# Optimization experiments

Hardware: AMD Instinct MI355X
Metric: run time of the kernel (lower is better)

## Reference

```python
import jax, jax.numpy as jnp
import numpy as np
import math

SEQ_LEN = 1024
NUM_FILTERS = 24
INPUT_DIM = 256
OUTPUT_DIM = 256
BATCH = 4


def _spectral_filters(seq_len, K):
    # Hankel matrix Z[i,j] = 2 / ((i+j)^3 - (i+j)), i,j in 1..L (use_hankel_L=False)
    entries = np.arange(1, seq_len + 1, dtype=np.float64)
    ipj = entries[:, None] + entries[None, :]
    Z = 2.0 / (ipj ** 3 - ipj)
    sigma, phi = np.linalg.eigh(Z)
    phi_k = phi[:, -K:] * (sigma[-K:] ** 0.25)
    return jnp.asarray(phi_k, dtype=jnp.float32)  # [L, K]


def setup_inputs() -> dict:
    key = jax.random.key(0)
    k1, k2, k3 = jax.random.split(key, 3)
    scale = (NUM_FILTERS * INPUT_DIM) ** (-0.5)
    x = jax.random.normal(k1, (BATCH, SEQ_LEN, INPUT_DIM), dtype=jnp.float32)
    phi = _spectral_filters(SEQ_LEN, NUM_FILTERS)
    M_phi_plus = jax.random.normal(k2, (NUM_FILTERS, INPUT_DIM, OUTPUT_DIM), dtype=jnp.float32) * scale
    M_phi_minus = jax.random.normal(k3, (NUM_FILTERS, INPUT_DIM, OUTPUT_DIM), dtype=jnp.float32) * scale
    return {"x": x, "phi": phi, "M_phi_plus": M_phi_plus, "M_phi_minus": M_phi_minus}


def reference(x, phi, M_phi_plus, M_phi_minus):
    B, L, I = x.shape
    n = 1 << math.ceil(math.log2(2 * L - 1))  # FFT length (2048 for L=1024)
    # alternating sign: +1 at even positions, -1 at odd (sgn[:,1::2] *= -1)
    sgn = jnp.where(jnp.arange(L) % 2 == 1, -1.0, 1.0).astype(jnp.float32)
    # FFT of filters: [F, K]
    V = jnp.fft.rfft(phi.astype(jnp.float32), n=n, axis=0)
    # FFT of input and sign-modulated input: [B, F, I]
    X = jnp.fft.rfft(x, n=n, axis=1)
    Xs = jnp.fft.rfft(x * sgn[None, :, None], n=n, axis=1)
    # pointwise multiply in frequency, broadcast over K: [B, F, K, I]
    U_plus = jnp.fft.irfft(V[None, :, :, None] * X[:, :, None, :], n=n, axis=1)[:, :L]
    U_minus = jnp.fft.irfft(V[None, :, :, None] * Xs[:, :, None, :], n=n, axis=1)[:, :L]
    U_minus = U_minus * sgn[None, :, None, None]
    # spectral projection: [B, L, O]
    out = jnp.einsum('blki,kio->blo', U_plus, M_phi_plus)
    out = out + jnp.einsum('blki,kio->blo', U_minus, M_phi_minus)
    return out
```

## Files before the change

### kernel.cpp

```cpp
#include <hip/hip_runtime.h>


#define ZB_ 12582912

typedef __attribute__((ext_vector_type(8))) short bf16x8;
typedef __attribute__((ext_vector_type(4))) float f32x4;

__device__ inline unsigned short f2bf(float f) {
    unsigned u = __float_as_uint(f);
    u += 0x7FFFu + ((u >> 16) & 1u);
    return (unsigned short)(u >> 16);
}

__device__ inline float bf2f(unsigned short s) {
    unsigned u = ((unsigned)s) << 16;
    return __uint_as_float(u);
}

__device__ inline void gl16(const unsigned short* g, unsigned short* l) {
    __builtin_amdgcn_global_load_lds((const __attribute__((address_space(1))) void*)g,
                                     (__attribute__((address_space(3))) void*)l, 16, 0, 0);
}

__global__ __launch_bounds__(256) void k_prep_all(const float* __restrict__ x,
                                                  const float* __restrict__ phi,
                                                  const float* __restrict__ Mp,
                                                  const float* __restrict__ Mm,
                                                  unsigned short* __restrict__ xb,
                                                  unsigned short* __restrict__ ToepA,
                                                  unsigned short* __restrict__ MbT) {
    __shared__ float tile[32][33];
    int bid = blockIdx.x, tid = threadIdx.x;
    if (bid < 1024) {
        int i = (bid * 256 + tid) * 4;
        float4 v = *(const float4*)(x + i);
        ushort4 o;
        o.x = f2bf(v.x); o.y = f2bf(v.y); o.z = f2bf(v.z); o.w = f2bf(v.w);
        int row = i >> 8, col = i & 255;
        int dst = (row << 8) | (col & 224) | ((col & 31) ^ (((row >> 1) & 3) << 3));
        *(ushort4*)(xb + dst) = o;
    } else if (bid < 1792) {
        int r = bid - 1024;
        int kk = r >> 4;
        int dm = (r & 15) - 1;
        int k = (kk < 24) ? kk : kk - 24;
        int i = tid >> 1, j0 = (tid & 1) * 32;
        unsigned short* dst = ToepA + ((size_t)kk * 16 + (dm + 1)) * 8192 + i * 64;
        int sw = (i & 7) << 3;
#pragma unroll
        for (int q = 0; q < 8; ++q) {
            int j = j0 + q * 4;
            unsigned short e[4];
#pragma unroll
            for (int ee = 0; ee < 4; ++ee) {
                int t = dm * 64 + i - (j + ee);
                float v = 0.f;
                if (t >= 0 && t < 1024) {
                    v = phi[t * 24 + k];
                    if (kk >= 24 && (t & 1)) v = -v;
                }
                e[ee] = f2bf(v);
            }
            ushort4 ov; ov.x = e[0]; ov.y = e[1]; ov.z = e[2]; ov.w = e[3];
            *(ushort4*)(dst + (j ^ sw)) = ov;
        }
    } else {
        int flat = bid - 1792;
        int kk = flat >> 6, rr = flat & 63;
        int i0 = (rr >> 3) * 32, o0 = (rr & 7) * 32;
        int tx = tid & 31, ty = tid >> 5;
        const float* src = ((kk < 24) ? Mp : Mm) + (size_t)((kk < 24) ? kk : kk - 24) * 65536;
        for (int j = 0; j < 4; ++j)
            tile[ty + j * 8][tx] = src[(i0 + ty + j * 8) * 256 + o0 + tx];
        __syncthreads();
        for (int j = 0; j < 4; ++j) {
            int orow = o0 + ty + j * 8, i = i0 + tx;
            int ic = (i & 224) | ((i & 31) ^ (((orow >> 1) & 3) << 3));
            MbT[(size_t)kk * 65536 + orow * 256 + ic] = f2bf(tile[tx][ty + j * 8]);
        }
    }
}

__global__ __launch_bounds__(256, 4) void k_stage1(const unsigned short* __restrict__ xb0,
                                                   const unsigned short* __restrict__ MbT,
                                                   unsigned short* __restrict__ Z) {
    __shared__ unsigned short Ab[2][4096];
    __shared__ unsigned short Bb[3][4096];
    int tid = threadIdx.x, lane = tid & 63, w = tid >> 6;
    int wm = w >> 1, wn = w & 1;

    int nwg = 768 * gridDim.z;
    int orig = blockIdx.x + blockIdx.y * 8 + blockIdx.z * 768;
    int wg = (orig & 7) * (nwg >> 3) + (orig >> 3);
    int m0 = (wg & 7) * 128;
    int rem = wg >> 3;
    int yy = rem % 96;
    int b  = rem / 96;
    int kk = yy >> 1;
    int o0 = (yy & 1) * 128;

    const unsigned short* xb_b = xb0 + (size_t)b * 262144;
    unsigned short* Zb = Z + (size_t)b * ZB_;
    const unsigned short* Bsrc = MbT + (size_t)kk * 65536;
    int l16 = lane & 15, kofs = (lane >> 4) * 8;
    int sw32 = ((l16 >> 1) & 3) << 3;
    int r4l = lane >> 2, c4 = (lane & 3) * 8;

    int arow[2], brow[2], lofs[2];
#pragma unroll
    for (int q = 0; q < 2; ++q) {
        int rr = q * 64 + w * 16 + r4l;
        arow[q] = (m0 + rr) * 256 + c4;
        brow[q] = (o0 + rr) * 256 + c4;
        lofs[q] = q * 2048 + w * 512;
    }

    f32x4 acc[4][4];
    for (int i = 0; i < 4; ++i)
        for (int j = 0; j < 4; ++j) {
            acc[i][j][0] = 0.f; acc[i][j][1] = 0.f; acc[i][j][2] = 0.f; acc[i][j][3] = 0.f;
        }

    auto stageA = [&](int bi, int ko) {
#pragma unroll
        for (int q = 0; q < 2; ++q) gl16(xb_b + arow[q] + ko * 32, &Ab[bi][0] + lofs[q]);
    };
    auto stageB = [&](int bi, int ko) {
#pragma unroll
        for (int q = 0; q < 2; ++q) gl16(Bsrc + brow[q] + ko * 32, &Bb[bi][0] + lofs[q]);
    };

    stageA(0, 0); stageB(0, 0); stageB(1, 1);

    for (int ko = 0; ko < 8; ++ko) {
        if (ko < 7) { asm volatile("s_waitcnt vmcnt(2)" ::: "memory"); }
        else        { asm volatile("s_waitcnt vmcnt(0)" ::: "memory"); }
        __builtin_amdgcn_sched_barrier(0);
        __builtin_amdgcn_s_barrier();
        __builtin_amdgcn_sched_barrier(0);
        if (ko < 7) stageA((ko + 1) & 1, ko + 1);
        if (ko < 6) stageB((ko + 2) % 3, ko + 2);

        const unsigned short* Abase = &Ab[ko & 1][0];
        const unsigned short* Bbase = &Bb[ko % 3][0];
        int koX = kofs ^ sw32;
        bf16x8 af[4], bfv[4];
#pragma unroll
        for (int mi = 0; mi < 4; ++mi)
            af[mi] = *(const bf16x8*)(Abase + (wm * 64 + mi * 16 + l16) * 32 + koX);
#pragma unroll
        for (int ni = 0; ni < 4; ++ni)
            bfv[ni] = *(const bf16x8*)(Bbase + (wn * 64 + ni * 16 + l16) * 32 + koX);
        __builtin_amdgcn_s_setprio(1);
#pragma unroll
        for (int mi = 0; mi < 4; ++mi)
#pragma unroll
            for (int ni = 0; ni < 4; ++ni)
                acc[mi][ni] = __builtin_amdgcn_mfma_f32_16x16x32_bf16(af[mi], bfv[ni], acc[mi][ni], 0, 0, 0);
        __builtin_amdgcn_s_setprio(0);
    }

    int r4 = (lane >> 4) * 4;
    for (int mi = 0; mi < 4; ++mi) {
        int sbase = m0 + wm * 64 + mi * 16 + r4;
        for (int ni = 0; ni < 4; ++ni) {
            int o = o0 + wn * 64 + ni * 16 + l16;
            ushort4 pk;
            pk.x = f2bf(acc[mi][ni][0]); pk.y = f2bf(acc[mi][ni][1]);
            pk.z = f2bf(acc[mi][ni][2]); pk.w = f2bf(acc[mi][ni][3]);
            *(ushort4*)(Zb + (size_t)kk * 262144 + (size_t)o * 1024 + (sbase ^ ((o & 7) << 3))) = pk;
        }
    }
}

__global__ __launch_bounds__(256, 2) void k_stage2(const unsigned short* __restrict__ Z,
                                                   const unsigned short* __restrict__ ToepA,
                                                   unsigned short* __restrict__ partial, int kkpg) {
    __shared__ unsigned short Abuf[2][8192];
    __shared__ unsigned short Zbuf[3][8192];
    int tid = threadIdx.x, lane = tid & 63, w = tid >> 6;
    int wm = w >> 1, wn = w & 1;

    int gy = gridDim.y, nwg = 4 * gy * gridDim.z;
    int orig = blockIdx.x + blockIdx.y * 4 + blockIdx.z * 4 * gy;
    int wg = (orig & 7) * (nwg >> 3) + (orig >> 3);
    int pr = wg & 3;
    int yy = (wg >> 2) % gy;
    int zz = (wg >> 2) / gy;
    int o0 = (yy & 1) * 128;
    int b  = yy >> 1;
    int kgi = zz;
    int kk0 = kgi * kkpg;

    int l16 = lane & 15, kofs = (lane >> 4) * 8;
    int sw = (l16 & 7) << 3;
    int r8 = lane >> 3, cg = lane & 7;

    const unsigned short* Zb = Z + (size_t)b * ZB_;
    unsigned short* pb = partial + ((size_t)b * gridDim.z + kgi) * 262144;

    int arow[4], zrow[4], lofs[4];
#pragma unroll
    for (int q = 0; q < 4; ++q) {
        int rr = q * 32 + w * 8 + r8;
        arow[q] = rr * 64 + cg * 8;
        zrow[q] = (o0 + rr) * 1024 + cg * 8;
        lofs[q] = q * 2048 + w * 512;
    }

    for (int half = 0; half < 2; ++half) {
        int lb = half ? (7 - pr) : pr;
        int l0 = lb * 128;
        int nch = 2 * lb + 2;
        int total = kkpg * nch;

        f32x4 acc[4][4];
        for (int i = 0; i < 4; ++i)
            for (int j = 0; j < 4; ++j) {
                acc[i][j][0] = 0.f; acc[i][j][1] = 0.f; acc[i][j][2] = 0.f; acc[i][j][3] = 0.f;
            }

        __syncthreads();

        auto stageA = [&](int bi, int kka, int didx) {
            const unsigned short* gA = ToepA + ((size_t)kka * 16 + didx) * 8192;
#pragma unroll
            for (int q = 0; q < 4; ++q) gl16(gA + arow[q], &Abuf[bi][0] + lofs[q]);
        };
        auto stageZ = [&](int bi, int kka, int s0) {
            const unsigned short* gZ = Zb + (size_t)kka * 262144 + s0;
#pragma unroll
            for (int q = 0; q < 4; ++q) gl16(gZ + zrow[q], &Zbuf[bi][0] + lofs[q]);
        };
        auto compute = [&](int ba, int bz) {
            const unsigned short* Abase = &Abuf[ba][0];
            const unsigned short* Zbase = &Zbuf[bz][0];
            __builtin_amdgcn_s_setprio(1);
#pragma unroll
            for (int ks = 0; ks < 2; ++ks) {
                int koX = (ks * 32 + kofs) ^ sw;
                bf16x8 af[4], bfv[4];
#pragma unroll
                for (int mi = 0; mi < 4; ++mi)
                    af[mi] = *(const bf16x8*)(Abase + (wm * 64 + mi * 16 + l16) * 64 + koX);
#pragma unroll
                for (int ni = 0; ni < 4; ++ni)
                    bfv[ni] = *(const bf16x8*)(Zbase + (wn * 64 + ni * 16 + l16) * 64 + koX);
#pragma unroll
                for (int mi = 0; mi < 4; ++mi)
#pragma unroll
                    for (int ni = 0; ni < 4; ++ni)
                        acc[mi][ni] = __builtin_amdgcn_mfma_f32_16x16x32_bf16(af[mi], bfv[ni], acc[mi][ni], 0, 0, 0);
            }
            __builtin_amdgcn_s_setprio(0);
        };

        stageA(0, kk0, 2 * lb + 1);
        stageZ(0, kk0, 0);
        stageZ(1, kk0, 64);

        int scA = 1, kkA = 0;
        int scZ = 2, kkZ = 0;
        if (scZ == nch) { scZ = 0; kkZ = 1; }
        int jz = 2;

        for (int j = 0; j < total - 1; ++j) {
            asm volatile("s_waitcnt vmcnt(4)" ::: "memory");
            __builtin_amdgcn_sched_barrier(0);
            __builtin_amdgcn_s_barrier();
            __builtin_amdgcn_sched_barrier(0);
            stageA((j + 1) & 1, kk0 + kkA, 2 * lb - scA + 1);
            ++scA; if (scA == nch) { scA = 0; ++kkA; }
            if (jz < total) {
                stageZ(jz % 3, kk0 + kkZ, scZ * 64);
                ++scZ; if (scZ == nch) { scZ = 0; ++kkZ; }
                ++jz;
            }
            compute(j & 1, j % 3);
        }
        asm volatile("s_waitcnt vmcnt(0)" ::: "memory");
        __builtin_amdgcn_sched_barrier(0);
        __builtin_amdgcn_s_barrier();
        __builtin_amdgcn_sched_barrier(0);
        compute((total - 1) & 1, (total - 1) % 3);

        int r4 = (lane >> 4) * 4;
        for (int mi = 0; mi < 4; ++mi) {
            int l = l0 + wm * 64 + mi * 16 + r4;
            for (int ni = 0; ni < 4; ++ni) {
                int o = o0 + wn * 64 + ni * 16 + l16;
                unsigned short* dst = pb + (size_t)l * 256 + o;
                dst[0]   = f2bf(acc[mi][ni][0]);
                dst[256] = f2bf(acc[mi][ni][1]);
                dst[512] = f2bf(acc[mi][ni][2]);
                dst[768] = f2bf(acc[mi][ni][3]);
            }
        }
    }
}

__global__ void k_reduce(const unsigned short* __restrict__ partial, float* __restrict__ outg, int kg) {
    const unsigned short* pb = partial + (size_t)blockIdx.y * kg * 262144;
    int i = (blockIdx.x * 256 + threadIdx.x) * 8;
    float s[8];
#pragma unroll
    for (int j = 0; j < 8; ++j) s[j] = 0.f;
    for (int kgi = 0; kgi < kg; ++kgi) {
        uint4 v = *(const uint4*)(pb + (size_t)kgi * 262144 + i);
        unsigned vv[4] = {v.x, v.y, v.z, v.w};
#pragma unroll
        for (int q = 0; q < 4; ++q) {
            s[q * 2]     += bf2f((unsigned short)(vv[q] & 0xFFFF));
            s[q * 2 + 1] += bf2f((unsigned short)(vv[q] >> 16));
        }
    }
    float4 o0, o1;
    o0.x = s[0]; o0.y = s[1]; o0.z = s[2]; o0.w = s[3];
    o1.x = s[4]; o1.y = s[5]; o1.z = s[6]; o1.w = s[7];
    float* dst = outg + (size_t)blockIdx.y * 262144 + i;
    *(float4*)(dst) = o0;
    *(float4*)(dst + 4) = o1;
}

extern "C" void kernel_launch(void* const* d_in, const int* in_sizes, int n_in,
                              void* d_out, int out_size, void* d_ws, size_t ws_size,
                              hipStream_t stream) {
    const float* x   = (const float*)d_in[0];
    const float* phi = (const float*)d_in[1];
    const float* Mp  = (const float*)d_in[2];
    const float* Mm  = (const float*)d_in[3];
    float* out = (float*)d_out;

    char* ws = (char*)d_ws;
    unsigned short* xb    = (unsigned short*)(ws);
    unsigned short* MbT   = (unsigned short*)(ws + 2097152);
    unsigned short* ToepA = (unsigned short*)(ws + 8388608);
    unsigned short* Zbuf  = (unsigned short*)(ws + 20971520);
    const size_t fixed = 20971520;

    int g = 4, kg = 16;
    auto need = [&](int gg, int kk) {
        return fixed + (size_t)gg * 25165824 + (size_t)gg * (size_t)kk * 524288;
    };
    if (need(4, 16) > ws_size) {
        kg = 12;
        if (need(4, 12) > ws_size) {
            g = 2; kg = 16;
            if (need(2, 16) > ws_size) {
                kg = 12;
                if (need(2, 12) > ws_size) {
                    g = 1; kg = 16;
                    if (need(1, 16) > ws_size) {
                        kg = 12;
                        if (need(1, 12) > ws_size) kg = 6;
                    }
                }
            }
        }
    }
    unsigned short* partial = (unsigned short*)(ws + fixed + (size_t)g * 25165824);

    k_prep_all<<<dim3(4864), dim3(256), 0, stream>>>(x, phi, Mp, Mm, xb, ToepA, MbT);

    for (int b0 = 0; b0 < 4; b0 += g) {
        k_stage1<<<dim3(8, 96, g), dim3(256), 0, stream>>>(xb + (size_t)b0 * 262144, MbT, Zbuf);
        k_stage2<<<dim3(4, 2 * g, kg), dim3(256), 0, stream>>>(Zbuf, ToepA, partial, 48 / kg);
        k_reduce<<<dim3(128, g), dim3(256), 0, stream>>>(partial, out + (size_t)b0 * 262144, kg);
    }
}
```

Baseline: 130.7 us.

## Halve stage-2 K-chunk to 32 with new swizzle, raise occupancy and split-K

The Toeplitz filter blocks are rebuilt as 128x32 tiles at 32-sample diagonal offsets, replacing the 128x64 tiles. The Z layout swizzle is changed to match, and stage 2 now streams 32-wide K chunks with half the LDS per buffer. This allows 4 workgroups per CU instead of 2, and the default split-K count rises from 16 to 24. The aim is higher occupancy, finer-grained triangular work and more parallelism, at the cost of more barriers per unit of work and more partial-sum traffic in the reduce step.

```diff
diff --git a/kernel.cpp b/kernel.cpp
--- a/kernel.cpp
+++ b/kernel.cpp
@@ -39,25 +39,27 @@
         int row = i >> 8, col = i & 255;
         int dst = (row << 8) | (col & 224) | ((col & 31) ^ (((row >> 1) & 3) << 3));
         *(ushort4*)(xb + dst) = o;
-    } else if (bid < 1792) {
+    } else if (bid < 2560) {
         int r = bid - 1024;
-        int kk = r >> 4;
-        int dm = (r & 15) - 1;
+        int kk = r >> 5;
+        int didx = r & 31;
+        int d = 32 * didx - 96;
         int k = (kk < 24) ? kk : kk - 24;
-        int i = tid >> 1, j0 = (tid & 1) * 32;
-        unsigned short* dst = ToepA + ((size_t)kk * 16 + (dm + 1)) * 8192 + i * 64;
-        int sw = (i & 7) << 3;
-#pragma unroll
-        for (int q = 0; q < 8; ++q) {
+        bool neg = kk >= 24;
+        int i = tid >> 1, j0 = (tid & 1) * 16;
+        unsigned short* dst = ToepA + ((size_t)kk * 32 + didx) * 4096 + i * 32;
+        int sw = ((i >> 1) & 3) << 3;
+#pragma unroll
+        for (int q = 0; q < 4; ++q) {
             int j = j0 + q * 4;
             unsigned short e[4];
 #pragma unroll
             for (int ee = 0; ee < 4; ++ee) {
-                int t = dm * 64 + i - (j + ee);
+                int t = d + i - (j + ee);
                 float v = 0.f;
                 if (t >= 0 && t < 1024) {
                     v = phi[t * 24 + k];
-                    if (kk >= 24 && (t & 1)) v = -v;
+                    if (neg && (t & 1)) v = -v;
                 }
                 e[ee] = f2bf(v);
             }
@@ -65,7 +67,7 @@
             *(ushort4*)(dst + (j ^ sw)) = ov;
         }
     } else {
-        int flat = bid - 1792;
+        int flat = bid - 2560;
         int kk = flat >> 6, rr = flat & 63;
         int i0 = (rr >> 3) * 32, o0 = (rr & 7) * 32;
         int tx = tid & 31, ty = tid >> 5;
@@ -161,23 +163,26 @@
     }
 
     int r4 = (lane >> 4) * 4;
+    int swo = 0;
     for (int mi = 0; mi < 4; ++mi) {
         int sbase = m0 + wm * 64 + mi * 16 + r4;
         for (int ni = 0; ni < 4; ++ni) {
             int o = o0 + wn * 64 + ni * 16 + l16;
+            swo = ((o >> 1) & 3) << 3;
+            int sidx = (sbase & ~31) | ((sbase & 31) ^ swo);
             ushort4 pk;
             pk.x = f2bf(acc[mi][ni][0]); pk.y = f2bf(acc[mi][ni][1]);
             pk.z = f2bf(acc[mi][ni][2]); pk.w = f2bf(acc[mi][ni][3]);
-            *(ushort4*)(Zb + (size_t)kk * 262144 + (size_t)o * 1024 + (sbase ^ ((o & 7) << 3))) = pk;
-        }
-    }
-}
-
-__global__ __launch_bounds__(256, 2) void k_stage2(const unsigned short* __restrict__ Z,
+            *(ushort4*)(Zb + (size_t)kk * 262144 + (size_t)o * 1024 + sidx) = pk;
+        }
+    }
+}
+
+__global__ __launch_bounds__(256, 4) void k_stage2(const unsigned short* __restrict__ Z,
                                                    const unsigned short* __restrict__ ToepA,
                                                    unsigned short* __restrict__ partial, int kkpg) {
-    __shared__ unsigned short Abuf[2][8192];
-    __shared__ unsigned short Zbuf[3][8192];
+    __shared__ unsigned short Abuf[2][4096];
+    __shared__ unsigned short Zbuf[3][4096];
     int tid = threadIdx.x, lane = tid & 63, w = tid >> 6;
     int wm = w >> 1, wn = w & 1;
 
@@ -193,25 +198,18 @@
     int kk0 = kgi * kkpg;
 
     int l16 = lane & 15, kofs = (lane >> 4) * 8;
-    int sw = (l16 & 7) << 3;
-    int r8 = lane >> 3, cg = lane & 7;
+    int koX = kofs ^ (((l16 >> 1) & 3) << 3);
 
     const unsigned short* Zb = Z + (size_t)b * ZB_;
     unsigned short* pb = partial + ((size_t)b * gridDim.z + kgi) * 262144;
 
-    int arow[4], zrow[4], lofs[4];
-#pragma unroll
-    for (int q = 0; q < 4; ++q) {
-        int rr = q * 32 + w * 8 + r8;
-        arow[q] = rr * 64 + cg * 8;
-        zrow[q] = (o0 + rr) * 1024 + cg * 8;
-        lofs[q] = q * 2048 + w * 512;
-    }
+    int t8 = tid * 8;
+    int zr = (tid >> 2) * 1024 + (tid & 3) * 8;
 
     for (int half = 0; half < 2; ++half) {
         int lb = half ? (7 - pr) : pr;
         int l0 = lb * 128;
-        int nch = 2 * lb + 2;
+        int nch = 4 * lb + 4;
         int total = kkpg * nch;
 
         f32x4 acc[4][4];
@@ -222,57 +220,52 @@
 
         __syncthreads();
 
-        auto stageA = [&](int bi, int kka, int didx) {
-            const unsigned short* gA = ToepA + ((size_t)kka * 16 + didx) * 8192;
-#pragma unroll
-            for (int q = 0; q < 4; ++q) gl16(gA + arow[q], &Abuf[bi][0] + lofs[q]);
+        auto stageA = [&](int bi, int kka, int sc) {
+            const unsigned short* gA = ToepA + ((size_t)kka * 32 + (4 * lb - sc + 3)) * 4096;
+            gl16(gA + t8, &Abuf[bi][0] + t8);
+            gl16(gA + 2048 + t8, &Abuf[bi][0] + 2048 + t8);
         };
-        auto stageZ = [&](int bi, int kka, int s0) {
-            const unsigned short* gZ = Zb + (size_t)kka * 262144 + s0;
-#pragma unroll
-            for (int q = 0; q < 4; ++q) gl16(gZ + zrow[q], &Zbuf[bi][0] + lofs[q]);
+        auto stageZ = [&](int bi, int kka, int sc) {
+            const unsigned short* gZ = Zb + (size_t)kka * 262144 + (size_t)o0 * 1024 + sc * 32;
+            gl16(gZ + zr, &Zbuf[bi][0] + t8);
+            gl16(gZ + 65536 + zr, &Zbuf[bi][0] + 2048 + t8);
         };
         auto compute = [&](int ba, int bz) {
             const unsigned short* Abase = &Abuf[ba][0];
             const unsigned short* Zbase = &Zbuf[bz][0];
+            bf16x8 af[4], bfv[4];
+#pragma unroll
+            for (int mi = 0; mi < 4; ++mi)
+                af[mi] = *(const bf16x8*)(Abase + (wm * 64 + mi * 16 + l16) * 32 + koX);
+#pragma unroll
+            for (int ni = 0; ni < 4; ++ni)
+                bfv[ni] = *(const bf16x8*)(Zbase + (wn * 64 + ni * 16 + l16) * 32 + koX);
             __builtin_amdgcn_s_setprio(1);
 #pragma unroll
-            for (int ks = 0; ks < 2; ++ks) {
-                int koX = (ks * 32 + kofs) ^ sw;
-                bf16x8 af[4], bfv[4];
-#pragma unroll
-                for (int mi = 0; mi < 4; ++mi)
-                    af[mi] = *(const bf16x8*)(Abase + (wm * 64 + mi * 16 + l16) * 64 + koX);
+            for (int mi = 0; mi < 4; ++mi)
 #pragma unroll
                 for (int ni = 0; ni < 4; ++ni)
-                    bfv[ni] = *(const bf16x8*)(Zbase + (wn * 64 + ni * 16 + l16) * 64 + koX);
-#pragma unroll
-                for (int mi = 0; mi < 4; ++mi)
-#pragma unroll
-                    for (int ni = 0; ni < 4; ++ni)
-                        acc[mi][ni] = __builtin_amdgcn_mfma_f32_16x16x32_bf16(af[mi], bfv[ni], acc[mi][ni], 0, 0, 0);
-            }
+                    acc[mi][ni] = __builtin_amdgcn_mfma_f32_16x16x32_bf16(af[mi], bfv[ni], acc[mi][ni], 0, 0, 0);
             __builtin_amdgcn_s_setprio(0);
         };
 
-        stageA(0, kk0, 2 * lb + 1);
+        stageA(0, kk0, 0);
         stageZ(0, kk0, 0);
-        stageZ(1, kk0, 64);
+        stageZ(1, kk0, 1);
 
         int scA = 1, kkA = 0;
         int scZ = 2, kkZ = 0;
-        if (scZ == nch) { scZ = 0; kkZ = 1; }
         int jz = 2;
 
         for (int j = 0; j < total - 1; ++j) {
-            asm volatile("s_waitcnt vmcnt(4)" ::: "memory");
+            asm volatile("s_waitcnt vmcnt(2)" ::: "memory");
             __builtin_amdgcn_sched_barrier(0);
             __builtin_amdgcn_s_barrier();
             __builtin_amdgcn_sched_barrier(0);
-            stageA((j + 1) & 1, kk0 + kkA, 2 * lb - scA + 1);
+            stageA((j + 1) & 1, kk0 + kkA, scA);
             ++scA; if (scA == nch) { scA = 0; ++kkA; }
             if (jz < total) {
-                stageZ(jz % 3, kk0 + kkZ, scZ * 64);
+                stageZ(jz % 3, kk0 + kkZ, scZ);
                 ++scZ; if (scZ == nch) { scZ = 0; ++kkZ; }
                 ++jz;
             }
@@ -338,21 +331,24 @@
     unsigned short* Zbuf  = (unsigned short*)(ws + 20971520);
     const size_t fixed = 20971520;
 
-    int g = 4, kg = 16;
+    int g = 4, kg = 24;
     auto need = [&](int gg, int kk) {
         return fixed + (size_t)gg * 25165824 + (size_t)gg * (size_t)kk * 524288;
     };
-    if (need(4, 16) > ws_size) {
-        kg = 12;
-        if (need(4, 12) > ws_size) {
-            g = 2; kg = 16;
-            if (need(2, 16) > ws_size) {
-                kg = 12;
-                if (need(2, 12) > ws_size) {
-                    g = 1; kg = 16;
-                    if (need(1, 16) > ws_size) {
-                        kg = 12;
-                        if (need(1, 12) > ws_size) kg = 6;
+    if (need(4, 24) > ws_size) {
+        kg = 16;
+        if (need(4, 16) > ws_size) {
+            kg = 12;
+            if (need(4, 12) > ws_size) {
+                g = 2; kg = 24;
+                if (need(2, 24) > ws_size) {
+                    kg = 12;
+                    if (need(2, 12) > ws_size) {
+                        g = 1; kg = 24;
+                        if (need(1, 24) > ws_size) {
+                            kg = 12;
+                            if (need(1, 12) > ws_size) kg = 6;
+                        }
                     }
                 }
             }
@@ -360,7 +356,7 @@
     }
     unsigned short* partial = (unsigned short*)(ws + fixed + (size_t)g * 25165824);
 
-    k_prep_all<<<dim3(4864), dim3(256), 0, stream>>>(x, phi, Mp, Mm, xb, ToepA, MbT);
+    k_prep_all<<<dim3(5632), dim3(256), 0, stream>>>(x, phi, Mp, Mm, xb, ToepA, MbT);
 
     for (int b0 = 0; b0 < 4; b0 += g) {
         k_stage1<<<dim3(8, 96, g), dim3(256), 0, stream>>>(xb + (size_t)b0 * 262144, MbT, Zbuf);
```

Result: slower. 134.1 us (+2.6%).
